# Optimization experiments

Measured on AMD Instinct MI355X. Metric: run time of the kernel, lower is better.

## Reference

```python
import jax, jax.numpy as jnp
import numpy as np

WS = (3, 8, 8)          # (t, h, w) window
SHIFT = (0, 4, 4)
HEADS = 6
DIM = 120
HD = DIM // HEADS
SCALE = HD ** -0.5
N = WS[0] * WS[1] * WS[2]   # 192 tokens per window
NQ = N // 3                 # 64 query tokens (last frame)


def _rel_pos_index():
    cd, ch, cw = np.arange(WS[0]), np.arange(WS[1]), np.arange(WS[2])
    c2 = np.stack(np.meshgrid(cd, ch, cw, indexing='ij')).reshape(3, -1)      # (3, N)
    c1 = np.stack(np.meshgrid(np.arange(1), ch, cw, indexing='ij')).reshape(3, -1)  # (3, NQ)
    rel = (c1[:, :, None] - c2[:, None, :]).transpose(1, 2, 0)                # (NQ, N, 3)
    rel = rel + np.array([WS[0] - 1, WS[1] - 1, WS[2] - 1])
    idx = rel[..., 0] * (2 * WS[1] - 1) * (2 * WS[2] - 1) + rel[..., 1] * (2 * WS[2] - 1) + rel[..., 2]
    return idx.astype(np.int32)  # values in [0, 3*15*15)


def _shift_attn_mask(h, w):
    # standard Swin shifted-window mask, tiled over the 3 frames
    img = np.zeros((h, w), np.int32)
    cnt = 0
    for hs in (slice(0, -WS[1]), slice(-WS[1], -SHIFT[1]), slice(-SHIFT[1], None)):
        for ws_ in (slice(0, -WS[2]), slice(-WS[2], -SHIFT[2]), slice(-SHIFT[2], None)):
            img[hs, ws_] = cnt
            cnt += 1
    win = img.reshape(h // WS[1], WS[1], w // WS[2], WS[2]).transpose(0, 2, 1, 3).reshape(-1, WS[1] * WS[2])
    m2 = win[:, None, :] - win[:, :, None]
    m2 = np.where(m2 != 0, -100.0, 0.0).astype(np.float32)  # (nW, 64, 64)
    return np.tile(m2, (1, 3, 3))                            # (nW, 192, 192)


def setup_inputs() -> dict:
    key = jax.random.key(0)
    ks = jax.random.split(key, 10)
    b, t, h, w, c = 1, 3, 256, 256, DIM
    nW = (h // WS[1]) * (w // WS[2])
    B_ = b * nW
    return {
        'x': jax.random.normal(ks[0], (b, t, h, w, c), jnp.float32),
        'quary0': jax.random.normal(ks[1], (B_, NQ, c), jnp.float32),
        'quary1': jax.random.normal(ks[2], (B_, NQ, c), jnp.float32),
        'qkv_w': jax.random.normal(ks[3], (3 * c, c), jnp.float32) * 0.02,
        'qkv_b': jnp.zeros((3 * c,), jnp.float32),
        'proj_w': jax.random.normal(ks[4], (c, c), jnp.float32) * 0.02,
        'proj_b': jnp.zeros((c,), jnp.float32),
        'rpb_table': jax.random.normal(ks[5], (WS[0] * (2 * WS[1] - 1) * (2 * WS[2] - 1), HEADS), jnp.float32) * 0.02,
        'pm_w': jax.random.normal(ks[6], (1, c), jnp.float32) * 0.02,
        'pm_b': jnp.zeros((1,), jnp.float32),
        'attn_mask': jnp.asarray(_shift_attn_mask(h, w)),
        'rel_idx': jnp.asarray(_rel_pos_index()),
    }


def reference(x, quary0, quary1, qkv_w, qkv_b, proj_w, proj_b, rpb_table, pm_w, pm_b, attn_mask, rel_idx):
    b, t, h, w, c = x.shape
    # cyclic shift
    x = jnp.roll(x, (-SHIFT[0], -SHIFT[1], -SHIFT[2]), axis=(1, 2, 3))
    # window partition -> (B_, N, c)
    xw = x.reshape(b, t // WS[0], WS[0], h // WS[1], WS[1], w // WS[2], WS[2], c)
    xw = xw.transpose(0, 1, 3, 5, 2, 4, 6, 7).reshape(-1, N, c)
    B_ = xw.shape[0]
    # adaptive mask prediction (eval path: hard threshold; sigmoid(s/T)>=0.5 <=> s>=0)
    pred_q = jax.lax.stop_gradient(xw[:, 2 * NQ:, :])
    soft = jnp.abs(pred_q - quary0) @ pm_w.T + pm_b          # (B_, NQ, 1)
    pred = (soft >= 0).astype(x.dtype)
    # qkv
    qkv = (xw @ qkv_w.T + qkv_b).reshape(B_, N, 3, HEADS, HD).transpose(2, 0, 3, 1, 4)
    q = qkv[0][:, :, 2 * NQ:, :] * SCALE                      # (B_, H, NQ, hd)
    k, v = qkv[1], qkv[2]                                     # (B_, H, N, hd)
    attn = jnp.einsum('bhqd,bhkd->bhqk', q, k)                # (B_, H, NQ, N)
    # gathered relative position bias
    rpb = rpb_table[rel_idx.reshape(-1)].reshape(NQ, N, HEADS).transpose(2, 0, 1)
    attn = attn + rpb[None]
    # shift mask
    nW = attn_mask.shape[0]
    attn = attn.reshape(b, nW, HEADS, NQ, N) + attn_mask[None, :, None, 2 * NQ:, :]
    attn = jax.nn.softmax(attn.reshape(B_, HEADS, NQ, N), axis=-1)
    out = jnp.einsum('bhqk,bhkd->bqhd', attn, v).reshape(B_, NQ, c)
    # output projection + token-pruning blend (math-equivalent to gather/fill eval path)
    x1 = out @ proj_w.T + proj_b
    x_pred = x1 * pred + quary1 * (1.0 - pred)
    xo = jnp.concatenate([x_pred, pred], axis=-1)             # (B_, NQ, c+1)
    # single-frame window reverse
    xo = xo.reshape(b, h // WS[1], w // WS[2], WS[1], WS[2], c + 1)
    xo = xo.transpose(0, 1, 3, 2, 4, 5).reshape(b, h, w, c + 1)
    xo = jnp.roll(xo, (SHIFT[1], SHIFT[2]), axis=(1, 2))
    return xo
```

## Files before the change

### kernel.cpp

```cpp
#include <hip/hip_runtime.h>
#include <math.h>

typedef __attribute__((ext_vector_type(8))) short s16x8;
typedef __attribute__((ext_vector_type(4))) float f32x4;

#define MFMA(a, b, c) __builtin_amdgcn_mfma_f32_16x16x32_bf16(a, b, c, 0, 0, 0)

#define KVF_OFF  0ull
#define QF_OFF   98304ull
#define PJF_OFF  147456ull
#define RPB_OFF  180224ull
#define KG_OFF   475136ull
#define QG_OFF   57098368ull
#define VT_OFF   82264192ull
#define PRED_OFF 129458304ull

__device__ __forceinline__ unsigned short f2bf(float f) {
    union { float f; unsigned int i; } v; v.f = f;
    unsigned int x = v.i;
    x += 0x7fffu + ((x >> 16) & 1u);
    return (unsigned short)(x >> 16);
}

__global__ void prep(const float* __restrict__ qkv_w,
                     const float* __restrict__ proj_w,
                     const float* __restrict__ rpb_table,
                     const int*   __restrict__ rel_idx,
                     unsigned char* __restrict__ wsb)
{
    int gid = blockIdx.x * blockDim.x + threadIdx.x;
    int nthr = gridDim.x * blockDim.x;
    unsigned short* KVF = (unsigned short*)(wsb + KVF_OFF);
    unsigned short* QF  = (unsigned short*)(wsb + QF_OFF);
    unsigned short* PJF = (unsigned short*)(wsb + PJF_OFF);
    float*          RPB = (float*)(wsb + RPB_OFF);

    for (int f = gid; f < 6 * 4 * 4 * 512; f += nthr) {
        int q = f & 511, rest = f >> 9;
        int kk = rest & 3, rest2 = rest >> 2;
        int nt = rest2 & 3, h = rest2 >> 2;
        int ln = q >> 3, j = q & 7;
        int l15 = ln & 15, qd = ln >> 4;
        int k = kk * 32 + qd * 8 + j;
        float v = 0.f;
        if (k < 120) {
            if (nt < 2) { int d = nt * 16 + l15;       if (d < 20) v = qkv_w[(120 + h * 20 + d) * 120 + k]; }
            else        { int d = (nt - 2) * 16 + l15; if (d < 20) v = qkv_w[(240 + h * 20 + d) * 120 + k]; }
        }
        KVF[f] = f2bf(v);
    }
    for (int f = gid; f < 6 * 2 * 4 * 512; f += nthr) {
        int q = f & 511, rest = f >> 9;
        int kk = rest & 3, rest2 = rest >> 2;
        int nt = rest2 & 1, h = rest2 >> 1;
        int ln = q >> 3, j = q & 7;
        int l15 = ln & 15, qd = ln >> 4;
        int nn = nt * 16 + l15, k = kk * 32 + qd * 8 + j;
        float v = (k < 120 && nn < 20) ? qkv_w[(h * 20 + nn) * 120 + k] : 0.f;
        QF[f] = f2bf(v);
    }
    for (int f = gid; f < 8 * 4 * 512; f += nthr) {
        int q = f & 511, rest = f >> 9;
        int kk = rest & 3, nt = rest >> 2;
        int ln = q >> 3, j = q & 7;
        int l15 = ln & 15, qd = ln >> 4;
        int c = nt * 16 + l15, k = kk * 32 + qd * 8 + j;
        float v = (k < 120 && c < 120) ? proj_w[c * 120 + k] : 0.f;
        PJF[f] = f2bf(v);
    }
    for (int i = gid; i < 6 * 64 * 192; i += nthr) {
        int n = i % 192, r = (i / 192) % 64, h = i / (192 * 64);
        RPB[i] = rpb_table[rel_idx[r * 192 + n] * 6 + h];
    }
}

__global__ __launch_bounds__(256, 3)
void k_qkv(const float* __restrict__ x, const float* __restrict__ quary0,
           const float* __restrict__ qkv_b, const float* __restrict__ pm_w,
           const float* __restrict__ pm_b, unsigned char* __restrict__ wsb)
{
    alignas(16) __shared__ unsigned short xw[192 * 120 + 16];
    const int tid = threadIdx.x;
    const int wv = tid >> 6, ln = tid & 63, l15 = ln & 15, qd = ln >> 4;
    const int widx = blockIdx.x, wh = widx >> 5, ww = widx & 31;
    const unsigned short* KVF = (const unsigned short*)(wsb + KVF_OFF);
    const unsigned short* QF  = (const unsigned short*)(wsb + QF_OFF);
    unsigned short* KG = (unsigned short*)(wsb + KG_OFF);
    unsigned short* QG = (unsigned short*)(wsb + QG_OFF);
    unsigned short* VT = (unsigned short*)(wsb + VT_OFF);
    float* PREDG = (float*)(wsb + PRED_OFF);

    for (int e = tid; e < 192 * 30; e += 256) {
        int n = e / 30, c4 = e % 30;
        int f = n >> 6, ii = (n >> 3) & 7, jj = n & 7;
        int y0 = (wh * 8 + ii + 4) & 255;
        int x0 = (ww * 8 + jj + 4) & 255;
        float4 val = *(const float4*)(x + (((size_t)(f * 256 + y0)) * 256 + x0) * 120 + c4 * 4);
        unsigned int lo = (unsigned)f2bf(val.x) | ((unsigned)f2bf(val.y) << 16);
        unsigned int hi = (unsigned)f2bf(val.z) | ((unsigned)f2bf(val.w) << 16);
        unsigned int off = (unsigned)(n * 120 + c4 * 4);
        *(unsigned int*)(xw + off)     = lo;
        *(unsigned int*)(xw + off + 2) = hi;
    }
    if (tid < 16) xw[192 * 120 + tid] = 0;
    {
        int r = tid >> 2, j = tid & 3;
        int ii = r >> 3, jj = r & 7;
        int y0 = (wh * 8 + ii + 4) & 255;
        int x0 = (ww * 8 + jj + 4) & 255;
        const float* xr  = x + (((size_t)(2 * 256 + y0)) * 256 + x0) * 120;
        const float* q0r = quary0 + ((size_t)widx * 64 + r) * 120;
        float acc = 0.f;
        for (int ch = j * 30; ch < j * 30 + 30; ++ch)
            acc += fabsf(xr[ch] - q0r[ch]) * pm_w[ch];
        acc += __shfl_xor(acc, 1);
        acc += __shfl_xor(acc, 2);
        if (j == 0) PREDG[widx * 64 + r] = (acc + pm_b[0] >= 0.f) ? 1.f : 0.f;
    }
    __syncthreads();

    const float SCALE = 0.22360679774997896f;
    for (int e = wv; e < 336; e += 4) {
        int mt, h, nt;
        const unsigned short *arow, *bb;
        bool isq = (e >= 288);
        if (!isq) {
            int ntg = e % 24; mt = e / 24; h = ntg >> 2; nt = ntg & 3;
            arow = xw + (mt * 16 + l15) * 120;
            bb = KVF + (size_t)((h * 4 + nt) * 4) * 512 + ln * 8;
        } else {
            int t = e - 288; int ntg = t % 12; mt = t / 12; h = ntg >> 1; nt = ntg & 1;
            arow = xw + (128 + mt * 16 + l15) * 120;
            bb = QF + (size_t)((h * 2 + nt) * 4) * 512 + ln * 8;
        }
        f32x4 acc = {0.f, 0.f, 0.f, 0.f};
        #pragma unroll
        for (int kk = 0; kk < 4; ++kk) {
            s16x8 aF = *(const s16x8*)(arow + kk * 32 + qd * 8);
            s16x8 bF = *(const s16x8*)(bb + kk * 512);
            acc = MFMA(aF, bF, acc);
        }
        if (!isq) {
            if (nt < 2) {
                int d = nt * 16 + l15;
                if (d < 24) {
                    float b = (d < 20) ? qkv_b[120 + h * 20 + d] : 0.f;
                    #pragma unroll
                    for (int reg = 0; reg < 4; ++reg) {
                        int tok = mt * 16 + qd * 4 + reg;
                        KG[((size_t)widx * 192 + tok) * 144 + h * 24 + d] = f2bf(acc[reg] + b);
                    }
                }
            } else {
                int d = (nt - 2) * 16 + l15;
                if (d < 20) {
                    float b = qkv_b[240 + h * 20 + d];
                    #pragma unroll
                    for (int reg = 0; reg < 4; ++reg) {
                        int tok = mt * 16 + qd * 4 + reg;
                        VT[((size_t)widx * 120 + h * 20 + d) * 192 + tok] = f2bf(acc[reg] + b);
                    }
                }
            }
        } else {
            int nn = nt * 16 + l15;
            float b = (nn < 20) ? qkv_b[h * 20 + nn] : 0.f;
            #pragma unroll
            for (int reg = 0; reg < 4; ++reg) {
                int row = mt * 16 + qd * 4 + reg;
                float v = (nn < 20) ? (acc[reg] + b) * SCALE : 0.f;
                QG[((size_t)widx * 64 + row) * 192 + h * 32 + nn] = f2bf(v);
            }
        }
    }
}

__global__ __launch_bounds__(384, 4)
void k_attn(const float* __restrict__ quary1, const float* __restrict__ proj_b,
            const unsigned char* __restrict__ wsb, float* __restrict__ out)
{
    alignas(16) __shared__ unsigned short ps[6 * 16 * 200];
    alignas(16) __shared__ unsigned short os[64 * 136];
    const int tid = threadIdx.x;
    const int h = tid >> 6, ln = tid & 63, l15 = ln & 15, qd = ln >> 4;
    const int widx = blockIdx.x, wh = widx >> 5, ww = widx & 31;

    const unsigned short* KG  = (const unsigned short*)(wsb + KG_OFF);
    const unsigned short* QG  = (const unsigned short*)(wsb + QG_OFF);
    const unsigned short* VT  = (const unsigned short*)(wsb + VT_OFF);
    const unsigned short* PJF = (const unsigned short*)(wsb + PJF_OFF);
    const float*          RPB = (const float*)(wsb + RPB_OFF);
    const float*        PREDG = (const float*)(wsb + PRED_OFF);

    for (int e = tid; e < 64 * 8; e += 384) os[(e >> 3) * 136 + 120 + (e & 7)] = 0;

    int gk[12];
    #pragma unroll
    for (int t = 0; t < 12; ++t) {
        int p = (t * 16 + l15) & 63;
        int hg = (wh == 31) ? (1 + ((p >> 3) >= 4)) : 0;
        int wg = (ww == 31) ? (1 + ((p & 7) >= 4)) : 0;
        gk[t] = hg * 3 + wg;
    }

    unsigned short* psw = ps + h * 16 * 200;
    const unsigned short* kbase = KG + (size_t)widx * 192 * 144 + h * 24 + qd * 8;
    const unsigned short* vbase = VT + ((size_t)widx * 120 + h * 20) * 192 + qd * 8;

    for (int rt = 0; rt < 4; ++rt) {
        const int rb = rt * 16;
        f32x4 sc[12];
        s16x8 qf = *(const s16x8*)(QG + ((size_t)widx * 64 + rb + l15) * 192 + h * 32 + qd * 8);
        #pragma unroll
        for (int t = 0; t < 12; ++t) {
            s16x8 bF = *(const s16x8*)(kbase + (size_t)(t * 16 + l15) * 144);
            f32x4 z = {0.f, 0.f, 0.f, 0.f};
            sc[t] = MFMA(qf, bF, z);
        }
        #pragma unroll
        for (int reg = 0; reg < 4; ++reg) {
            int row = rb + qd * 4 + reg;
            int hgq = (wh == 31) ? (1 + ((row >> 3) >= 4)) : 0;
            int wgq = (ww == 31) ? (1 + ((row & 7) >= 4)) : 0;
            int gq = hgq * 3 + wgq;
            const float* rr = RPB + ((size_t)(h * 64 + row)) * 192;
            float m = -1e30f;
            #pragma unroll
            for (int t = 0; t < 12; ++t) {
                float v = sc[t][reg] + rr[t * 16 + l15] + ((gq == gk[t]) ? 0.f : -100.f);
                sc[t][reg] = v; m = fmaxf(m, v);
            }
            m = fmaxf(m, __shfl_xor(m, 1));
            m = fmaxf(m, __shfl_xor(m, 2));
            m = fmaxf(m, __shfl_xor(m, 4));
            m = fmaxf(m, __shfl_xor(m, 8));
            float s = 0.f;
            #pragma unroll
            for (int t = 0; t < 12; ++t) {
                float ev = __expf(sc[t][reg] - m);
                sc[t][reg] = ev; s += ev;
            }
            s += __shfl_xor(s, 1);
            s += __shfl_xor(s, 2);
            s += __shfl_xor(s, 4);
            s += __shfl_xor(s, 8);
            float inv = 1.0f / s;
            #pragma unroll
            for (int t = 0; t < 12; ++t)
                psw[(qd * 4 + reg) * 200 + t * 16 + l15] = f2bf(sc[t][reg] * inv);
        }
        f32x4 a0 = {0.f, 0.f, 0.f, 0.f}, a1 = {0.f, 0.f, 0.f, 0.f};
        #pragma unroll
        for (int kk = 0; kk < 6; ++kk) {
            s16x8 pF = *(const s16x8*)(psw + l15 * 200 + kk * 32 + qd * 8);
            s16x8 v0 = *(const s16x8*)(vbase + (size_t)l15 * 192 + kk * 32);
            s16x8 v1 = *(const s16x8*)(vbase + (size_t)(16 + l15) * 192 + kk * 32);
            a0 = MFMA(v0, pF, a0);
            a1 = MFMA(v1, pF, a1);
        }
        #pragma unroll
        for (int reg = 0; reg < 4; ++reg) {
            os[(rb + l15) * 136 + h * 20 + qd * 4 + reg] = f2bf(a0[reg]);
            if (qd == 0) os[(rb + l15) * 136 + h * 20 + 16 + reg] = f2bf(a1[reg]);
        }
    }
    __syncthreads();

    for (int e = h; e < 32; e += 6) {
        int mt = e & 3, nt = e >> 2;
        int c = nt * 16 + l15;
        f32x4 acc = {0.f, 0.f, 0.f, 0.f};
        #pragma unroll
        for (int kk = 0; kk < 4; ++kk) {
            s16x8 aF = *(const s16x8*)(os + (mt * 16 + l15) * 136 + kk * 32 + qd * 8);
            s16x8 bF = *(const s16x8*)(PJF + (size_t)((nt * 4 + kk) * 512) + ln * 8);
            acc = MFMA(aF, bF, acc);
        }
        if (c < 120) {
            float pb = proj_b[c];
            #pragma unroll
            for (int reg = 0; reg < 4; ++reg) {
                int r = mt * 16 + qd * 4 + reg;
                float p = PREDG[widx * 64 + r];
                int ii = r >> 3, jj = r & 7;
                int y0 = (wh * 8 + ii + 4) & 255;
                int x0 = (ww * 8 + jj + 4) & 255;
                float fin = (p != 0.f) ? (acc[reg] + pb)
                                       : quary1[(size_t)widx * 7680 + (size_t)r * 120 + c];
                out[((size_t)(y0 * 256 + x0)) * 121 + c] = fin;
            }
        }
    }
    if (tid < 64) {
        int r = tid;
        int ii = r >> 3, jj = r & 7;
        int y0 = (wh * 8 + ii + 4) & 255;
        int x0 = (ww * 8 + jj + 4) & 255;
        out[((size_t)(y0 * 256 + x0)) * 121 + 120] = PREDG[widx * 64 + r];
    }
}

extern "C" void kernel_launch(void* const* d_in, const int* in_sizes, int n_in,
                              void* d_out, int out_size, void* d_ws, size_t ws_size,
                              hipStream_t stream) {
    const float* x        = (const float*)d_in[0];
    const float* quary0   = (const float*)d_in[1];
    const float* quary1   = (const float*)d_in[2];
    const float* qkv_w    = (const float*)d_in[3];
    const float* qkv_b    = (const float*)d_in[4];
    const float* proj_w   = (const float*)d_in[5];
    const float* proj_b   = (const float*)d_in[6];
    const float* rpb      = (const float*)d_in[7];
    const float* pm_w     = (const float*)d_in[8];
    const float* pm_b     = (const float*)d_in[9];
    const int*   rel_idx  = (const int*)d_in[11];
    float* out = (float*)d_out;
    unsigned char* wsb = (unsigned char*)d_ws;

    prep<<<256, 256, 0, stream>>>(qkv_w, proj_w, rpb, rel_idx, wsb);
    k_qkv<<<1024, 256, 0, stream>>>(x, quary0, qkv_b, pm_w, pm_b, wsb);
    k_attn<<<1024, 384, 0, stream>>>(quary1, proj_b, wsb, out);
}
```

Before: 529.0 us.

## Restructure QKV projection into weight-stationary strips with head-major K/Q layouts

The projection loop now has each wave keep one weight strip in registers and sweep all token tiles, instead of reloading B fragments for every tile. The V projection swaps its MFMA operands so the transposed V stores run contiguously along tokens. K and Q in global memory become head-major (per window and head, contiguous rows of 24/32), which shortens strides for the attention kernel's loads. The cost is more register pressure, plus changed global layouts that the consumer kernel has to match.

```diff
diff --git a/kernel.cpp b/kernel.cpp
--- a/kernel.cpp
+++ b/kernel.cpp
@@ -120,57 +120,79 @@
     __syncthreads();
 
     const float SCALE = 0.22360679774997896f;
-    for (int e = wv; e < 336; e += 4) {
-        int mt, h, nt;
-        const unsigned short *arow, *bb;
-        bool isq = (e >= 288);
-        if (!isq) {
-            int ntg = e % 24; mt = e / 24; h = ntg >> 2; nt = ntg & 3;
-            arow = xw + (mt * 16 + l15) * 120;
-            bb = KVF + (size_t)((h * 4 + nt) * 4) * 512 + ln * 8;
-        } else {
-            int t = e - 288; int ntg = t % 12; mt = t / 12; h = ntg >> 1; nt = ntg & 1;
-            arow = xw + (128 + mt * 16 + l15) * 120;
-            bb = QF + (size_t)((h * 2 + nt) * 4) * 512 + ln * 8;
-        }
-        f32x4 acc = {0.f, 0.f, 0.f, 0.f};
-        #pragma unroll
-        for (int kk = 0; kk < 4; ++kk) {
-            s16x8 aF = *(const s16x8*)(arow + kk * 32 + qd * 8);
-            s16x8 bF = *(const s16x8*)(bb + kk * 512);
-            acc = MFMA(aF, bF, acc);
-        }
-        if (!isq) {
-            if (nt < 2) {
-                int d = nt * 16 + l15;
-                if (d < 24) {
-                    float b = (d < 20) ? qkv_b[120 + h * 20 + d] : 0.f;
-                    #pragma unroll
-                    for (int reg = 0; reg < 4; ++reg) {
-                        int tok = mt * 16 + qd * 4 + reg;
-                        KG[((size_t)widx * 192 + tok) * 144 + h * 24 + d] = f2bf(acc[reg] + b);
-                    }
-                }
-            } else {
-                int d = (nt - 2) * 16 + l15;
-                if (d < 20) {
-                    float b = qkv_b[240 + h * 20 + d];
-                    #pragma unroll
-                    for (int reg = 0; reg < 4; ++reg) {
-                        int tok = mt * 16 + qd * 4 + reg;
-                        VT[((size_t)widx * 120 + h * 20 + d) * 192 + tok] = f2bf(acc[reg] + b);
-                    }
-                }
-            }
-        } else {
-            int nn = nt * 16 + l15;
-            float b = (nn < 20) ? qkv_b[h * 20 + nn] : 0.f;
-            #pragma unroll
-            for (int reg = 0; reg < 4; ++reg) {
-                int row = mt * 16 + qd * 4 + reg;
-                float v = (nn < 20) ? (acc[reg] + b) * SCALE : 0.f;
-                QG[((size_t)widx * 64 + row) * 192 + h * 32 + nn] = f2bf(v);
-            }
+
+    for (int ksi = 0; ksi < 3; ++ksi) {
+        int strip = wv + ksi * 4;
+        int h = strip >> 1, nt = strip & 1;
+        const unsigned short* bb = KVF + (size_t)((h * 4 + nt) * 4) * 512 + ln * 8;
+        s16x8 b0 = *(const s16x8*)(bb);
+        s16x8 b1 = *(const s16x8*)(bb + 512);
+        s16x8 b2 = *(const s16x8*)(bb + 1024);
+        s16x8 b3 = *(const s16x8*)(bb + 1536);
+        int d = nt * 16 + l15;
+        float bias = (d < 20) ? qkv_b[120 + h * 20 + d] : 0.f;
+        for (int mt = 0; mt < 12; ++mt) {
+            const unsigned short* ar = xw + (mt * 16 + l15) * 120 + qd * 8;
+            f32x4 acc = {0.f, 0.f, 0.f, 0.f};
+            acc = MFMA(*(const s16x8*)(ar),      b0, acc);
+            acc = MFMA(*(const s16x8*)(ar + 32), b1, acc);
+            acc = MFMA(*(const s16x8*)(ar + 64), b2, acc);
+            acc = MFMA(*(const s16x8*)(ar + 96), b3, acc);
+            if (d < 24) {
+                size_t base = ((size_t)(widx * 6 + h) * 192 + mt * 16 + qd * 4) * 24 + d;
+                #pragma unroll
+                for (int reg = 0; reg < 4; ++reg)
+                    KG[base + reg * 24] = f2bf(acc[reg] + bias);
+            }
+        }
+    }
+
+    for (int vsi = 0; vsi < 3; ++vsi) {
+        int strip = wv + vsi * 4;
+        int h = strip >> 1, nt = strip & 1;
+        const unsigned short* bb = KVF + (size_t)((h * 4 + 2 + nt) * 4) * 512 + ln * 8;
+        s16x8 w0 = *(const s16x8*)(bb);
+        s16x8 w1 = *(const s16x8*)(bb + 512);
+        s16x8 w2 = *(const s16x8*)(bb + 1024);
+        s16x8 w3 = *(const s16x8*)(bb + 1536);
+        int drow = nt * 16 + qd * 4;
+        for (int mt = 0; mt < 12; ++mt) {
+            const unsigned short* ar = xw + (mt * 16 + l15) * 120 + qd * 8;
+            f32x4 acc = {0.f, 0.f, 0.f, 0.f};
+            acc = MFMA(w0, *(const s16x8*)(ar),      acc);
+            acc = MFMA(w1, *(const s16x8*)(ar + 32), acc);
+            acc = MFMA(w2, *(const s16x8*)(ar + 64), acc);
+            acc = MFMA(w3, *(const s16x8*)(ar + 96), acc);
+            if (drow < 20) {
+                size_t base = ((size_t)widx * 120 + h * 20 + drow) * 192 + mt * 16 + l15;
+                #pragma unroll
+                for (int reg = 0; reg < 4; ++reg)
+                    VT[base + (size_t)reg * 192] = f2bf(acc[reg] + qkv_b[240 + h * 20 + drow + reg]);
+            }
+        }
+    }
+
+    for (int qsi = 0; qsi < 3; ++qsi) {
+        int strip = wv + qsi * 4;
+        int h = strip >> 1, ntq = strip & 1;
+        const unsigned short* bb = QF + (size_t)((h * 2 + ntq) * 4) * 512 + ln * 8;
+        s16x8 b0 = *(const s16x8*)(bb);
+        s16x8 b1 = *(const s16x8*)(bb + 512);
+        s16x8 b2 = *(const s16x8*)(bb + 1024);
+        s16x8 b3 = *(const s16x8*)(bb + 1536);
+        int nn = ntq * 16 + l15;
+        float qb = (nn < 20) ? qkv_b[h * 20 + nn] : 0.f;
+        for (int mt = 0; mt < 4; ++mt) {
+            const unsigned short* ar = xw + (128 + mt * 16 + l15) * 120 + qd * 8;
+            f32x4 acc = {0.f, 0.f, 0.f, 0.f};
+            acc = MFMA(*(const s16x8*)(ar),      b0, acc);
+            acc = MFMA(*(const s16x8*)(ar + 32), b1, acc);
+            acc = MFMA(*(const s16x8*)(ar + 64), b2, acc);
+            acc = MFMA(*(const s16x8*)(ar + 96), b3, acc);
+            size_t base = ((size_t)(widx * 6 + h) * 64 + mt * 16 + qd * 4) * 32 + nn;
+            #pragma unroll
+            for (int reg = 0; reg < 4; ++reg)
+                QG[base + reg * 32] = f2bf((acc[reg] + qb) * SCALE);
         }
     }
 }
@@ -204,16 +226,17 @@
     }
 
     unsigned short* psw = ps + h * 16 * 200;
-    const unsigned short* kbase = KG + (size_t)widx * 192 * 144 + h * 24 + qd * 8;
+    const unsigned short* kbase = KG + (size_t)(widx * 6 + h) * 192 * 24 + qd * 8;
+    const unsigned short* qbase = QG + (size_t)(widx * 6 + h) * 64 * 32 + qd * 8;
     const unsigned short* vbase = VT + ((size_t)widx * 120 + h * 20) * 192 + qd * 8;
 
     for (int rt = 0; rt < 4; ++rt) {
         const int rb = rt * 16;
         f32x4 sc[12];
-        s16x8 qf = *(const s16x8*)(QG + ((size_t)widx * 64 + rb + l15) * 192 + h * 32 + qd * 8);
+        s16x8 qf = *(const s16x8*)(qbase + (size_t)(rb + l15) * 32);
         #pragma unroll
         for (int t = 0; t < 12; ++t) {
-            s16x8 bF = *(const s16x8*)(kbase + (size_t)(t * 16 + l15) * 144);
+            s16x8 bF = *(const s16x8*)(kbase + (size_t)(t * 16 + l15) * 24);
             f32x4 z = {0.f, 0.f, 0.f, 0.f};
             sc[t] = MFMA(qf, bF, z);
         }
```

After: 549.9 us. +3.9%, slower.
